# Kernel optimization log

Hardware: AMD Instinct MI355X
Metric: run time of the kernel (lower is better)

Reference implementation:

```python
import jax, jax.numpy as jnp
import numpy as np

EPS = 1e-20
TEMP = 0.07
HEAD_DIM = 128


def setup_inputs() -> dict:
    key = jax.random.key(0)
    k1, k2, k3 = jax.random.split(key, 3)
    B, C, T, H, W = 4, 512, 8, 32, 32
    x = jax.random.normal(k1, (B, C, T, H, W), dtype=jnp.float32)
    W_head = jax.random.normal(k2, (C, HEAD_DIM), dtype=jnp.float32) / np.sqrt(C).astype(np.float32)
    b_head = jax.random.normal(k3, (HEAD_DIM,), dtype=jnp.float32) * 0.01
    return {"x": x, "W_head": W_head, "b_head": b_head}


def _forward(x, W_head, b_head):
    B, C, T, H, W = x.shape
    N = H * W
    # linear head over channel dim (equivalent to permute->Linear->permute)
    feats = jnp.einsum('bcthw,cd->bdthw', x, W_head) + b_head[None, :, None, None, None]
    keys = feats.reshape(B, HEAD_DIM, T, N)
    # F.normalize(p=2, dim=1): x / max(||x||, 1e-12)
    norm = jnp.maximum(jnp.linalg.norm(keys, axis=1, keepdims=True), 1e-12)
    keys = keys / norm
    # affinity between consecutive frames: [B, T-1, N, N]
    A = jnp.einsum('bctn,bctm->btnm', keys[:, :, :-1], keys[:, :, 1:])
    A12 = jax.nn.softmax(A / TEMP, axis=-1)                         # forward stochastic mats
    A21 = jax.nn.softmax(jnp.swapaxes(A, -1, -2) / TEMP, axis=-1)   # backward stochastic mats
    A12s = jnp.swapaxes(A12, 0, 1)  # [T-1, B, N, N]
    A21s = jnp.swapaxes(A21, 0, 1)  # [T-1, B, N, N]

    # prefix products P[i] = A12[0] @ A12[1] @ ... @ A12[i]
    def step_p(carry, a):
        c = carry @ a
        return c, c
    _, Ptail = jax.lax.scan(step_p, A12s[0], A12s[1:])
    P = jnp.concatenate([A12s[:1], Ptail], axis=0)  # [T-1, B, N, N]

    # suffix products S[i] = A21[i] @ A21[i-1] @ ... @ A21[0]
    def step_s(carry, a):
        c = a @ carry
        return c, c
    _, Stail = jax.lax.scan(step_s, A21s[0], A21s[1:])
    S = jnp.concatenate([A21s[:1], Stail], axis=0)  # [T-1, B, N, N]

    # cycle walks for i = 1..T-2: aar_i = P[i] @ S[i]
    aars = jnp.matmul(P[1:], S[1:])  # [T-2, B, N, N]
    logits = jnp.log(aars + EPS)
    # cross-entropy with identity targets: loss = logsumexp - logit[n, n]
    lse = jax.nn.logsumexp(logits, axis=-1)                  # [T-2, B, N]
    diag = jnp.diagonal(logits, axis1=-2, axis2=-1)          # [T-2, B, N]
    losses = jnp.mean(lse - diag, axis=(1, 2))               # [T-2]
    preds = jnp.argmax(logits, axis=-1)                      # [T-2, B, N]
    tgt = jnp.arange(N)[None, None, :]
    accs = jnp.mean((preds == tgt).astype(jnp.float32), axis=(1, 2))
    # original returns (loss_of_last_walk, diags); diags exposed as stacked arrays
    return losses[-1], losses, accs


def reference(x, W_head, b_head):
    return _forward(x, W_head, b_head)
```

## Files before the change

kernel.cpp:

```cpp
#include <hip/hip_runtime.h>
#include <cstdint>
#include <cstddef>

typedef unsigned short u16;
typedef unsigned long long u64;
using short8 = __attribute__((ext_vector_type(8))) short;
using f32x4  = __attribute__((ext_vector_type(4))) float;

#define KEXP 20.609929155556620f

__device__ __forceinline__ u16 f2bf(float f) {
  unsigned u = __float_as_uint(f);
  u += 0x7fffu + ((u >> 16) & 1u);
  return (u16)(u >> 16);
}
__device__ __forceinline__ float bf2f(u16 h) { return __uint_as_float(((unsigned)h) << 16); }

typedef const unsigned int GASu32 __attribute__((address_space(1)));
typedef unsigned int LASu32 __attribute__((address_space(3)));

__device__ __forceinline__ void gload16(const u16* src, u16* dstLds) {
  __builtin_amdgcn_global_load_lds((GASu32*)src, (LASu32*)dstLds, 16, 0, 0);
}

__global__ __launch_bounds__(256) void transpose_x(const float* __restrict__ x, u16* __restrict__ xT) {
  __shared__ float t[32][33];
  int b = blockIdx.z, c0 = blockIdx.y * 32, s0 = blockIdx.x * 32;
  int tid = threadIdx.x;
  int ci = tid >> 3, s4 = (tid & 7) * 4;
  float4 v = *(const float4*)(x + ((size_t)b * 512 + c0 + ci) * 8192 + s0 + s4);
  t[ci][s4 + 0] = v.x; t[ci][s4 + 1] = v.y; t[ci][s4 + 2] = v.z; t[ci][s4 + 3] = v.w;
  __syncthreads();
  int si = tid >> 3, c4 = (tid & 7) * 4;
  ushort4 o;
  o.x = f2bf(t[c4 + 0][si]); o.y = f2bf(t[c4 + 1][si]);
  o.z = f2bf(t[c4 + 2][si]); o.w = f2bf(t[c4 + 3][si]);
  *(ushort4*)(xT + ((size_t)b * 8192 + s0 + si) * 512 + c0 + c4) = o;
}

__global__ __launch_bounds__(256) void transpose_w(const float* __restrict__ W, u16* __restrict__ Wt) {
  int idx = blockIdx.x * 256 + threadIdx.x;
  int d = idx >> 9, c = idx & 511;
  Wt[idx] = f2bf(W[c * 128 + d]);
}

__global__ __launch_bounds__(256) void normalize_keys(u16* __restrict__ keys) {
  int wv = threadIdx.x >> 6, lane = threadIdx.x & 63;
  int row = blockIdx.x * 4 + wv;
  unsigned* p = (unsigned*)(keys + (size_t)row * 128) + lane;
  unsigned v = *p;
  float a = bf2f((u16)(v & 0xffffu)), b = bf2f((u16)(v >> 16));
  float s = a * a + b * b;
  #pragma unroll
  for (int m = 1; m < 64; m <<= 1) s += __shfl_xor(s, m, 64);
  float sc = 1.f / fmaxf(sqrtf(s), 1e-12f);
  *p = (unsigned)f2bf(a * sc) | ((unsigned)f2bf(b * sc) << 16);
}

__global__ __launch_bounds__(256) void reduce_sums(const float* __restrict__ rsEP, const float* __restrict__ csEP,
                                                   float* __restrict__ rsumE, float* __restrict__ csumE) {
  int idx = blockIdx.x * 256 + threadIdx.x;
  int which = idx >= 28672;
  int base = which ? idx - 28672 : idx;
  int z = base >> 10, r = base & 1023;
  const float* src = which ? csEP : rsEP;
  float s = 0.f;
  #pragma unroll
  for (int k = 0; k < 16; ++k) s += src[(size_t)z * 16384 + k * 1024 + r];
  (which ? csumE : rsumE)[z * 1024 + r] = s;
}

__global__ __launch_bounds__(256) void k3_t0(const u16* __restrict__ E, const float* __restrict__ rsum,
                                             const float* __restrict__ csum,
                                             u16* __restrict__ P0, u16* __restrict__ S0) {
  int b = blockIdx.z, r = blockIdx.x;
  int zE = b * 7;
  const u16* e = E + ((size_t)zE << 20) + (size_t)r * 1024;
  float rr = 1.f / rsum[zE * 1024 + r];
  int c = threadIdx.x * 4;
  ushort4 v = *(const ushort4*)(e + c);
  float4 cv = *(const float4*)(csum + zE * 1024 + c);
  ushort4 o1, o2;
  float v0 = bf2f(v.x), v1 = bf2f(v.y), v2 = bf2f(v.z), v3 = bf2f(v.w);
  o1.x = f2bf(v0 * rr); o1.y = f2bf(v1 * rr); o1.z = f2bf(v2 * rr); o1.w = f2bf(v3 * rr);
  o2.x = f2bf(v0 / cv.x); o2.y = f2bf(v1 / cv.y); o2.z = f2bf(v2 / cv.z); o2.w = f2bf(v3 / cv.w);
  size_t base = ((size_t)b << 20) + (size_t)r * 1024 + c;
  *(ushort4*)(P0 + base) = o1;
  *(ushort4*)(S0 + base) = o2;
}

__global__ __launch_bounds__(256) void k3_tr(const u16* __restrict__ E, const float* __restrict__ rsum,
                                             const float* __restrict__ csum,
                                             u16* __restrict__ Bp, u16* __restrict__ Bs) {
  __shared__ u16 t[64][66];
  int z = blockIdx.z; int b = z / 6, tt = z % 6 + 1;
  int zE = b * 7 + tt;
  int er0 = blockIdx.x * 64, ec0 = blockIdx.y * 64;
  const u16* e = E + ((size_t)zE << 20);
  int tid = threadIdx.x;
  int ri = tid >> 4, c4 = (tid & 15) * 4;
  #pragma unroll
  for (int p = 0; p < 4; ++p) {
    ushort4 v = *(const ushort4*)(e + (size_t)(er0 + ri + p * 16) * 1024 + ec0 + c4);
    t[ri + p * 16][c4 + 0] = v.x; t[ri + p * 16][c4 + 1] = v.y;
    t[ri + p * 16][c4 + 2] = v.z; t[ri + p * 16][c4 + 3] = v.w;
  }
  __syncthreads();
  size_t outBase = (size_t)(b * 6 + tt - 1) << 20;
  float ir0 = 1.f / rsum[zE * 1024 + er0 + c4 + 0];
  float ir1 = 1.f / rsum[zE * 1024 + er0 + c4 + 1];
  float ir2 = 1.f / rsum[zE * 1024 + er0 + c4 + 2];
  float ir3 = 1.f / rsum[zE * 1024 + er0 + c4 + 3];
  #pragma unroll
  for (int p = 0; p < 4; ++p) {
    int roL = ri + p * 16;
    int ro = ec0 + roL;
    float ic = 1.f / csum[zE * 1024 + ro];
    float v0 = bf2f(t[c4 + 0][roL]), v1 = bf2f(t[c4 + 1][roL]);
    float v2 = bf2f(t[c4 + 2][roL]), v3 = bf2f(t[c4 + 3][roL]);
    ushort4 op, os;
    op.x = f2bf(v0 * ir0); op.y = f2bf(v1 * ir1); op.z = f2bf(v2 * ir2); op.w = f2bf(v3 * ir3);
    os.x = f2bf(v0 * ic);  os.y = f2bf(v1 * ic);  os.z = f2bf(v2 * ic);  os.w = f2bf(v3 * ic);
    size_t off = outBase + (size_t)ro * 1024 + er0 + c4;
    *(ushort4*)(Bp + off) = op;
    *(ushort4*)(Bs + off) = os;
  }
}

struct GemmBatch { const u16* A[24]; const u16* B[24]; u16* C[8]; };
enum { M_HEAD = 0, M_EXP = 1, M_PLAIN = 2, M_AAR = 3 };

__device__ __forceinline__ int lds_off32(int r, int kbyte) {
  int rp = r >> 1;
  int sl = (((r & 1) << 2) | (kbyte >> 4)) ^ (rp & 7);
  return rp * 128 + sl * 16;
}

#define GEMM_BODY(T, FA, FB, NA, NB)                                                    \
  {                                                                                     \
    int t_ = (T);                                                                       \
    if (t_ + 1 < nt) {                                                                  \
      if (t_ + 2 < nt) asm volatile("s_waitcnt vmcnt(4)" ::: "memory");                 \
      else             asm volatile("s_waitcnt vmcnt(0)" ::: "memory");                 \
      __builtin_amdgcn_s_barrier();                                                     \
      __builtin_amdgcn_sched_barrier(0);                                                \
      _Pragma("unroll")                                                                 \
      for (int f = 0; f < 4; ++f) {                                                     \
        NA[f] = *(const short8*)((const char*)An + offA[f]);                            \
        NB[f] = *(const short8*)((const char*)Bn + offB[f]);                            \
      }                                                                                 \
      if (t_ + 3 < nt) {                                                                \
        int k0_ = (t_ + 3) << 5;                                                        \
        gload16(srcA0 + k0_, A3 + ldso0);                                               \
        gload16(srcA1 + k0_, A3 + ldso1);                                               \
        gload16(srcB0 + k0_, B3 + ldso0);                                               \
        gload16(srcB1 + k0_, B3 + ldso1);                                               \
      }                                                                                 \
      asm volatile("s_waitcnt lgkmcnt(8)" ::: "memory");                                \
    } else {                                                                            \
      asm volatile("s_waitcnt lgkmcnt(0)" ::: "memory");                                \
    }                                                                                   \
    __builtin_amdgcn_sched_barrier(0);                                                  \
    __builtin_amdgcn_s_setprio(1);                                                      \
    _Pragma("unroll")                                                                   \
    for (int fr = 0; fr < 4; ++fr)                                                      \
      _Pragma("unroll")                                                                 \
      for (int fc2 = 0; fc2 < 4; ++fc2)                                                 \
        acc[fr][fc2] = __builtin_amdgcn_mfma_f32_16x16x32_bf16(FA[fr], FB[fc2],         \
                                                               acc[fr][fc2], 0, 0, 0); \
    __builtin_amdgcn_s_setprio(0);                                                      \
    { u16* tA = Ac; Ac = An; An = A2; A2 = A3; A3 = tA;                                 \
      u16* tB = Bc; Bc = Bn; Bn = B2; B2 = B3; B3 = tB; }                               \
  }

template <int MODE>
__global__ __launch_bounds__(256) void gemm_nt(const u16* __restrict__ gA, const u16* __restrict__ gB,
                                               u16* __restrict__ gC, GemmBatch batch,
                                               const float* __restrict__ bias,
                                               float* __restrict__ rsP, u64* __restrict__ amP,
                                               float* __restrict__ diagv,
                                               float* __restrict__ rsEP, float* __restrict__ csEP) {
  __shared__ u16 AsL[4][4096];
  __shared__ u16 BsL[4][4096];
  int tid = threadIdx.x, lane = tid & 63, wv = tid >> 6;
  int wr = wv >> 1, wc = wv & 1;
  int l15 = lane & 15, kb = (lane >> 4) << 4;

  int swz;
  { int per = (int)gridDim.x >> 3; int id0 = blockIdx.x; swz = (id0 & 7) * per + (id0 >> 3); }
  int z, m0, n0;
  if constexpr (MODE == M_HEAD) { z = 0; m0 = swz << 7; n0 = 0; }
  else { z = swz >> 6; int r6 = swz & 63; m0 = (r6 & 7) << 7; n0 = (r6 >> 3) << 7; }

  const u16 *A, *B; u16* C;
  int K, lda, ldb, ldc;
  if constexpr (MODE == M_HEAD) {
    A = gA; B = gB; C = gC; K = 512; lda = 512; ldb = 512; ldc = 128;
  } else if constexpr (MODE == M_EXP) {
    int b = z / 7, t = z % 7;
    size_t offA0 = (size_t)(b * 8 + t) * 131072;
    A = gA + offA0; B = gA + offA0 + 131072; C = gC + ((size_t)z << 20);
    K = 128; lda = 128; ldb = 128; ldc = 1024;
  } else if constexpr (MODE == M_PLAIN) {
    A = batch.A[z]; B = batch.B[z]; C = batch.C[z];
    K = 1024; lda = 1024; ldb = 1024; ldc = 1024;
  } else {
    A = batch.A[z]; B = batch.B[z]; C = nullptr;
    K = 1024; lda = 1024; ldb = 1024; ldc = 1024;
  }

  const u16 *srcA0, *srcA1, *srcB0, *srcB1;
  int ldso0, ldso1;
  {
    int g0 = tid, g1 = 256 + tid;
    int rp0 = g0 >> 3, sp0 = (g0 & 7) ^ (rp0 & 7);
    int r0_ = (rp0 << 1) | (sp0 >> 2), kb0 = (sp0 & 3) * 8;
    int rp1 = g1 >> 3, sp1 = (g1 & 7) ^ (rp1 & 7);
    int r1_ = (rp1 << 1) | (sp1 >> 2), kb1 = (sp1 & 3) * 8;
    srcA0 = A + (size_t)(m0 + r0_) * lda + kb0;
    srcA1 = A + (size_t)(m0 + r1_) * lda + kb1;
    srcB0 = B + (size_t)(n0 + r0_) * ldb + kb0;
    srcB1 = B + (size_t)(n0 + r1_) * ldb + kb1;
    ldso0 = g0 * 8; ldso1 = g1 * 8;
  }
  int offA[4], offB[4];
  #pragma unroll
  for (int f = 0; f < 4; ++f) {
    offA[f] = lds_off32((wr << 6) + (f << 4) + l15, kb);
    offB[f] = lds_off32((wc << 6) + (f << 4) + l15, kb);
  }

  f32x4 acc[4][4] = {};
  int nt = K >> 5;

  u16 *Ac = AsL[0], *An = AsL[1], *A2 = AsL[2], *A3 = AsL[3];
  u16 *Bc = BsL[0], *Bn = BsL[1], *B2 = BsL[2], *B3 = BsL[3];

  gload16(srcA0 +  0, Ac + ldso0); gload16(srcA1 +  0, Ac + ldso1);
  gload16(srcB0 +  0, Bc + ldso0); gload16(srcB1 +  0, Bc + ldso1);
  gload16(srcA0 + 32, An + ldso0); gload16(srcA1 + 32, An + ldso1);
  gload16(srcB0 + 32, Bn + ldso0); gload16(srcB1 + 32, Bn + ldso1);
  gload16(srcA0 + 64, A2 + ldso0); gload16(srcA1 + 64, A2 + ldso1);
  gload16(srcB0 + 64, B2 + ldso0); gload16(srcB1 + 64, B2 + ldso1);
  asm volatile("s_waitcnt vmcnt(8)" ::: "memory");
  __builtin_amdgcn_s_barrier();
  __builtin_amdgcn_sched_barrier(0);
  short8 fa0[4], fb0[4], fa1[4], fb1[4];
  #pragma unroll
  for (int f = 0; f < 4; ++f) {
    fa0[f] = *(const short8*)((const char*)Ac + offA[f]);
    fb0[f] = *(const short8*)((const char*)Bc + offB[f]);
  }

  for (int t = 0; t < nt; t += 2) {
    GEMM_BODY(t,     fa0, fb0, fa1, fb1);
    GEMM_BODY(t + 1, fa1, fb1, fa0, fb0);
  }

  if constexpr (MODE == M_AAR) {
    int nb = n0 >> 7;
    size_t pbase = (size_t)z * 16384 + (size_t)((nb << 1) | wc) * 1024;
    #pragma unroll
    for (int fr = 0; fr < 4; ++fr) {
      #pragma unroll
      for (int j = 0; j < 4; ++j) {
        float rs = 0.f, mv = -1.f; int mc = 0;
        #pragma unroll
        for (int fc = 0; fc < 4; ++fc) {
          float v = acc[fr][fc][j];
          rs += v;
          int c = n0 + (wc << 6) + (fc << 4) + l15;
          if (v > mv) { mv = v; mc = c; }
        }
        u64 pk = ((u64)__float_as_uint(mv) << 32) | (u64)(unsigned)(1023 - mc);
        #pragma unroll
        for (int m = 1; m < 16; m <<= 1) {
          rs += __shfl_xor(rs, m, 64);
          u64 o = __shfl_xor(pk, m, 64);
          pk = (o > pk) ? o : pk;
        }
        if (l15 == 0) {
          int row = m0 + (wr << 6) + (fr << 4) + ((lane >> 4) << 2) + j;
          rsP[pbase + row] = rs;
          amP[pbase + row] = pk;
        }
      }
      if (m0 == n0 && wr == wc) {
        int jj = l15 - ((lane >> 4) << 2);
        if (jj >= 0 && jj < 4) {
          int row = m0 + (wr << 6) + (fr << 4) + l15;
          float dv = (jj == 0) ? acc[fr][fr][0] : (jj == 1) ? acc[fr][fr][1]
                    : (jj == 2) ? acc[fr][fr][2] : acc[fr][fr][3];
          diagv[(z << 10) + row] = dv;
        }
      }
    }
  } else if constexpr (MODE == M_EXP) {
    float rp[4][4] = {};
    float cp[4] = {};
    #pragma unroll
    for (int fr = 0; fr < 4; ++fr)
      #pragma unroll
      for (int fc = 0; fc < 4; ++fc)
        #pragma unroll
        for (int j = 0; j < 4; ++j) {
          int row = m0 + (wr << 6) + (fr << 4) + ((lane >> 4) << 2) + j;
          int col = n0 + (wc << 6) + (fc << 4) + l15;
          float v = exp2f(acc[fr][fc][j] * KEXP);
          C[(size_t)row * ldc + col] = f2bf(v);
          rp[fr][j] += v;
          cp[fc] += v;
        }
    int nb = n0 >> 7, mb = m0 >> 7;
    size_t rbase = (size_t)z * 16384 + (size_t)((nb << 1) | wc) * 1024;
    size_t cbase = (size_t)z * 16384 + (size_t)((mb << 1) | wr) * 1024;
    #pragma unroll
    for (int fr = 0; fr < 4; ++fr)
      #pragma unroll
      for (int j = 0; j < 4; ++j) {
        float r = rp[fr][j];
        r += __shfl_xor(r, 1, 64); r += __shfl_xor(r, 2, 64);
        r += __shfl_xor(r, 4, 64); r += __shfl_xor(r, 8, 64);
        if (l15 == 0) {
          int row = m0 + (wr << 6) + (fr << 4) + ((lane >> 4) << 2) + j;
          rsEP[rbase + row] = r;
        }
      }
    #pragma unroll
    for (int fc = 0; fc < 4; ++fc) {
      float c = cp[fc];
      c += __shfl_xor(c, 16, 64); c += __shfl_xor(c, 32, 64);
      if ((lane >> 4) == 0) {
        int col = n0 + (wc << 6) + (fc << 4) + l15;
        csEP[cbase + col] = c;
      }
    }
  } else {
    #pragma unroll
    for (int fr = 0; fr < 4; ++fr)
      #pragma unroll
      for (int fc = 0; fc < 4; ++fc)
        #pragma unroll
        for (int j = 0; j < 4; ++j) {
          int row = m0 + (wr << 6) + (fr << 4) + ((lane >> 4) << 2) + j;
          int col = n0 + (wc << 6) + (fc << 4) + l15;
          float v = acc[fr][fc][j];
          if constexpr (MODE == M_HEAD) v += bias[col];
          C[(size_t)row * ldc + col] = f2bf(v);
        }
  }
}

__global__ __launch_bounds__(256) void finalize_k(const float* __restrict__ rsP, const u64* __restrict__ amP,
                                                  const float* __restrict__ diagv, float* __restrict__ out) {
  __shared__ float sl[256], sa[256];
  int w = blockIdx.x;
  int tid = threadIdx.x;
  float ls = 0.f, ac = 0.f;
  for (int idx = tid; idx < 4096; idx += 256) {
    int b = idx >> 10, n = idx & 1023;
    int z = (w << 2) + b;
    size_t base = (size_t)z * 16384 + n;
    float rs = 0.f; u64 pk = 0;
    #pragma unroll
    for (int k = 0; k < 16; ++k) {
      rs += rsP[base + k * 1024];
      u64 o = amP[base + k * 1024];
      pk = (o > pk) ? o : pk;
    }
    float dv = diagv[(z << 10) + n];
    ls += logf(rs + 1024.f * 1e-20f) - logf(dv + 1e-20f);
    unsigned pred = 1023u - (unsigned)(pk & 0xffffffffULL);
    ac += (pred == (unsigned)n) ? 1.f : 0.f;
  }
  sl[tid] = ls; sa[tid] = ac;
  __syncthreads();
  for (int s2 = 128; s2 > 0; s2 >>= 1) {
    if (tid < s2) { sl[tid] += sl[tid + s2]; sa[tid] += sa[tid + s2]; }
    __syncthreads();
  }
  if (tid == 0) {
    float loss = sl[0] / 4096.f, acv = sa[0] / 4096.f;
    out[1 + w] = loss;
    out[7 + w] = acv;
    if (w == 5) out[0] = loss;
  }
}

extern "C" void kernel_launch(void* const* d_in, const int* in_sizes, int n_in,
                              void* d_out, int out_size, void* d_ws, size_t ws_size,
                              hipStream_t stream) {
  (void)in_sizes; (void)n_in; (void)out_size; (void)ws_size;
  const float* x  = (const float*)d_in[0];
  const float* Wh = (const float*)d_in[1];
  const float* bh = (const float*)d_in[2];
  float* out = (float*)d_out;
  char* ws = (char*)d_ws;
  const size_t MB = 1ull << 20;

  u16* xT   = (u16*)(ws);
  u16* keys = (u16*)(ws + 32 * MB);
  float* rsP   = (float*)(ws + 32 * MB);
  u64*   amP   = (u64*)(ws + 34 * MB);
  float* diagv = (float*)(ws + 38 * MB);
  u16* Wt   = (u16*)(ws + 40 * MB);
  float* rsumE = (float*)(ws + 40 * MB + 128 * 1024);
  float* csumE = (float*)(ws + 40 * MB + 256 * 1024);
  u16* E    = (u16*)(ws + 41 * MB);
  float* rsEP  = (float*)(ws + 113 * MB);
  float* csEP  = (float*)(ws + 115 * MB);
  u16* Bp   = (u16*)(ws + 113 * MB);
  u16* Bs   = (u16*)(ws + 161 * MB);

  u16* Pb[7] = { (u16*)(ws + 97 * MB), (u16*)(ws + 0 * MB), (u16*)(ws + 8 * MB),
                 (u16*)(ws + 16 * MB), (u16*)(ws + 24 * MB), (u16*)(ws + 41 * MB),
                 (u16*)(ws + 49 * MB) };
  u16* Sb[7] = { (u16*)(ws + 105 * MB), (u16*)(ws + 57 * MB), (u16*)(ws + 65 * MB),
                 (u16*)(ws + 73 * MB), (u16*)(ws + 81 * MB), (u16*)(ws + 89 * MB),
                 (u16*)(ws + 97 * MB) };

  GemmBatch empty{};

  transpose_x<<<dim3(256, 16, 4), 256, 0, stream>>>(x, xT);
  transpose_w<<<dim3(256), 256, 0, stream>>>(Wh, Wt);
  gemm_nt<M_HEAD><<<dim3(256), 256, 0, stream>>>(xT, Wt, keys, empty, bh,
                                                 nullptr, nullptr, nullptr, nullptr, nullptr);
  normalize_keys<<<dim3(8192), 256, 0, stream>>>(keys);
  gemm_nt<M_EXP><<<dim3(1792), 256, 0, stream>>>(keys, nullptr, E, empty, nullptr,
                                                 nullptr, nullptr, nullptr, rsEP, csEP);
  reduce_sums<<<dim3(224), 256, 0, stream>>>(rsEP, csEP, rsumE, csumE);
  k3_t0<<<dim3(1024, 1, 4), 256, 0, stream>>>(E, rsumE, csumE, Pb[0], Sb[0]);
  k3_tr<<<dim3(16, 16, 24), 256, 0, stream>>>(E, rsumE, csumE, Bp, Bs);

  for (int i = 1; i <= 6; ++i) {
    GemmBatch gb{};
    for (int b = 0; b < 4; ++b) {
      gb.A[b]     = Pb[i - 1] + (size_t)b * 1048576;
      gb.B[b]     = Bp + (size_t)(b * 6 + i - 1) * 1048576;
      gb.C[b]     = Pb[i] + (size_t)b * 1048576;
      gb.A[4 + b] = Sb[i - 1] + (size_t)b * 1048576;
      gb.B[4 + b] = Bs + (size_t)(b * 6 + i - 1) * 1048576;
      gb.C[4 + b] = Sb[i] + (size_t)b * 1048576;
    }
    gemm_nt<M_PLAIN><<<dim3(512), 256, 0, stream>>>(nullptr, nullptr, nullptr, gb, nullptr,
                                                    nullptr, nullptr, nullptr, nullptr, nullptr);
  }

  GemmBatch ga{};
  for (int i = 1; i <= 6; ++i)
    for (int b = 0; b < 4; ++b) {
      ga.A[(i - 1) * 4 + b] = Pb[i] + (size_t)b * 1048576;
      ga.B[(i - 1) * 4 + b] = Sb[i] + (size_t)b * 1048576;
    }
  gemm_nt<M_AAR><<<dim3(1536), 256, 0, stream>>>(nullptr, nullptr, nullptr, ga, nullptr,
                                                 rsP, amP, diagv, nullptr, nullptr);
  finalize_k<<<dim3(6), 256, 0, stream>>>(rsP, amP, diagv, out);
}
```

Measured before the change: 320.6 us.

## Enlarge GEMM tiles to 256x256 with 512-thread blocks and triple buffering

The batched bf16 GEMM moves from 128x128 tiles on 4 waves to 256x256 tiles on 8 waves, with each wave computing 128x64 (8x4 MFMA fragments). The LDS pipeline drops from four stages to three so the larger tiles fit, and the epilogue indexing for the exp, row/col-sum, argmax and diagonal outputs is rewritten for the new layout. The column-sum partials and reduce_sums shrink to 8 partials, and the head GEMM pads W to 256 columns with zeros. The aim is more data reuse per loaded byte. The cost is fewer blocks (128 for the plain GEMMs on a 256-CU part), more registers per thread, and a shallower prefetch depth.

```diff
diff --git a/kernel.cpp b/kernel.cpp
--- a/kernel.cpp
+++ b/kernel.cpp
@@ -41,7 +41,7 @@
 __global__ __launch_bounds__(256) void transpose_w(const float* __restrict__ W, u16* __restrict__ Wt) {
   int idx = blockIdx.x * 256 + threadIdx.x;
   int d = idx >> 9, c = idx & 511;
-  Wt[idx] = f2bf(W[c * 128 + d]);
+  Wt[idx] = (d < 128) ? f2bf(W[c * 128 + d]) : (u16)0;
 }
 
 __global__ __launch_bounds__(256) void normalize_keys(u16* __restrict__ keys) {
@@ -60,14 +60,20 @@
 __global__ __launch_bounds__(256) void reduce_sums(const float* __restrict__ rsEP, const float* __restrict__ csEP,
                                                    float* __restrict__ rsumE, float* __restrict__ csumE) {
   int idx = blockIdx.x * 256 + threadIdx.x;
-  int which = idx >= 28672;
-  int base = which ? idx - 28672 : idx;
-  int z = base >> 10, r = base & 1023;
-  const float* src = which ? csEP : rsEP;
-  float s = 0.f;
-  #pragma unroll
-  for (int k = 0; k < 16; ++k) s += src[(size_t)z * 16384 + k * 1024 + r];
-  (which ? csumE : rsumE)[z * 1024 + r] = s;
+  if (idx < 28672) {
+    int z = idx >> 10, r = idx & 1023;
+    float s = 0.f;
+    #pragma unroll
+    for (int k = 0; k < 16; ++k) s += rsEP[(size_t)z * 16384 + k * 1024 + r];
+    rsumE[z * 1024 + r] = s;
+  } else {
+    int b2 = idx - 28672;
+    int z = b2 >> 10, c = b2 & 1023;
+    float s = 0.f;
+    #pragma unroll
+    for (int k = 0; k < 8; ++k) s += csEP[(size_t)z * 8192 + k * 1024 + c];
+    csumE[z * 1024 + c] = s;
+  }
 }
 
 __global__ __launch_bounds__(256) void k3_t0(const u16* __restrict__ E, const float* __restrict__ rsum,
@@ -145,52 +151,49 @@
       __builtin_amdgcn_s_barrier();                                                     \
       __builtin_amdgcn_sched_barrier(0);                                                \
       _Pragma("unroll")                                                                 \
-      for (int f = 0; f < 4; ++f) {                                                     \
-        NA[f] = *(const short8*)((const char*)An + offA[f]);                            \
-        NB[f] = *(const short8*)((const char*)Bn + offB[f]);                            \
-      }                                                                                 \
+      for (int f = 0; f < 8; ++f) NA[f] = *(const short8*)((const char*)An + offA[f]);  \
+      _Pragma("unroll")                                                                 \
+      for (int f = 0; f < 4; ++f) NB[f] = *(const short8*)((const char*)Bn + offB[f]);  \
       if (t_ + 3 < nt) {                                                                \
         int k0_ = (t_ + 3) << 5;                                                        \
-        gload16(srcA0 + k0_, A3 + ldso0);                                               \
-        gload16(srcA1 + k0_, A3 + ldso1);                                               \
-        gload16(srcB0 + k0_, B3 + ldso0);                                               \
-        gload16(srcB1 + k0_, B3 + ldso1);                                               \
+        gload16(sA0 + k0_, Ac + d0); gload16(sA1 + k0_, Ac + d1);                       \
+        gload16(sB0 + k0_, Bc + d0); gload16(sB1 + k0_, Bc + d1);                       \
       }                                                                                 \
-      asm volatile("s_waitcnt lgkmcnt(8)" ::: "memory");                                \
+      asm volatile("s_waitcnt lgkmcnt(12)" ::: "memory");                               \
     } else {                                                                            \
       asm volatile("s_waitcnt lgkmcnt(0)" ::: "memory");                                \
     }                                                                                   \
     __builtin_amdgcn_sched_barrier(0);                                                  \
     __builtin_amdgcn_s_setprio(1);                                                      \
     _Pragma("unroll")                                                                   \
-    for (int fr = 0; fr < 4; ++fr)                                                      \
+    for (int fa = 0; fa < 8; ++fa)                                                      \
       _Pragma("unroll")                                                                 \
-      for (int fc2 = 0; fc2 < 4; ++fc2)                                                 \
-        acc[fr][fc2] = __builtin_amdgcn_mfma_f32_16x16x32_bf16(FA[fr], FB[fc2],         \
-                                                               acc[fr][fc2], 0, 0, 0); \
+      for (int fb = 0; fb < 4; ++fb)                                                    \
+        acc[fa][fb] = __builtin_amdgcn_mfma_f32_16x16x32_bf16(FA[fa], FB[fb],           \
+                                                              acc[fa][fb], 0, 0, 0);   \
     __builtin_amdgcn_s_setprio(0);                                                      \
-    { u16* tA = Ac; Ac = An; An = A2; A2 = A3; A3 = tA;                                 \
-      u16* tB = Bc; Bc = Bn; Bn = B2; B2 = B3; B3 = tB; }                               \
+    { u16* tA = Ac; Ac = An; An = A2; A2 = tA;                                          \
+      u16* tB = Bc; Bc = Bn; Bn = B2; B2 = tB; }                                        \
   }
 
 template <int MODE>
-__global__ __launch_bounds__(256) void gemm_nt(const u16* __restrict__ gA, const u16* __restrict__ gB,
-                                               u16* __restrict__ gC, GemmBatch batch,
-                                               const float* __restrict__ bias,
-                                               float* __restrict__ rsP, u64* __restrict__ amP,
-                                               float* __restrict__ diagv,
-                                               float* __restrict__ rsEP, float* __restrict__ csEP) {
-  __shared__ u16 AsL[4][4096];
-  __shared__ u16 BsL[4][4096];
+__global__ __launch_bounds__(512, 2) void gemm_nt(const u16* __restrict__ gA, const u16* __restrict__ gB,
+                                                  u16* __restrict__ gC, GemmBatch batch,
+                                                  const float* __restrict__ bias,
+                                                  float* __restrict__ rsP, u64* __restrict__ amP,
+                                                  float* __restrict__ diagv,
+                                                  float* __restrict__ rsEP, float* __restrict__ csEP) {
+  __shared__ u16 AsL[3][8192];
+  __shared__ u16 BsL[3][8192];
   int tid = threadIdx.x, lane = tid & 63, wv = tid >> 6;
-  int wr = wv >> 1, wc = wv & 1;
+  int wrM = wv >> 2, wrN = wv & 3;
   int l15 = lane & 15, kb = (lane >> 4) << 4;
 
   int swz;
   { int per = (int)gridDim.x >> 3; int id0 = blockIdx.x; swz = (id0 & 7) * per + (id0 >> 3); }
   int z, m0, n0;
-  if constexpr (MODE == M_HEAD) { z = 0; m0 = swz << 7; n0 = 0; }
-  else { z = swz >> 6; int r6 = swz & 63; m0 = (r6 & 7) << 7; n0 = (r6 >> 3) << 7; }
+  if constexpr (MODE == M_HEAD) { z = 0; m0 = swz << 8; n0 = 0; }
+  else { z = swz >> 4; int r4 = swz & 15; m0 = (r4 & 3) << 8; n0 = (r4 >> 2) << 8; }
 
   const u16 *A, *B; u16* C;
   int K, lda, ldb, ldc;
@@ -209,48 +212,45 @@
     K = 1024; lda = 1024; ldb = 1024; ldc = 1024;
   }
 
-  const u16 *srcA0, *srcA1, *srcB0, *srcB1;
-  int ldso0, ldso1;
+  const u16 *sA0, *sA1, *sB0, *sB1;
+  int d0 = tid * 8, d1 = (512 + tid) * 8;
   {
-    int g0 = tid, g1 = 256 + tid;
+    int g0 = tid, g1 = 512 + tid;
     int rp0 = g0 >> 3, sp0 = (g0 & 7) ^ (rp0 & 7);
     int r0_ = (rp0 << 1) | (sp0 >> 2), kb0 = (sp0 & 3) * 8;
     int rp1 = g1 >> 3, sp1 = (g1 & 7) ^ (rp1 & 7);
     int r1_ = (rp1 << 1) | (sp1 >> 2), kb1 = (sp1 & 3) * 8;
-    srcA0 = A + (size_t)(m0 + r0_) * lda + kb0;
-    srcA1 = A + (size_t)(m0 + r1_) * lda + kb1;
-    srcB0 = B + (size_t)(n0 + r0_) * ldb + kb0;
-    srcB1 = B + (size_t)(n0 + r1_) * ldb + kb1;
-    ldso0 = g0 * 8; ldso1 = g1 * 8;
-  }
-  int offA[4], offB[4];
-  #pragma unroll
-  for (int f = 0; f < 4; ++f) {
-    offA[f] = lds_off32((wr << 6) + (f << 4) + l15, kb);
-    offB[f] = lds_off32((wc << 6) + (f << 4) + l15, kb);
-  }
-
-  f32x4 acc[4][4] = {};
+    sA0 = A + (size_t)(m0 + r0_) * lda + kb0;
+    sA1 = A + (size_t)(m0 + r1_) * lda + kb1;
+    sB0 = B + (size_t)(n0 + r0_) * ldb + kb0;
+    sB1 = B + (size_t)(n0 + r1_) * ldb + kb1;
+  }
+  int offA[8], offB[4];
+  #pragma unroll
+  for (int f = 0; f < 8; ++f) offA[f] = lds_off32(wrM * 128 + f * 16 + l15, kb);
+  #pragma unroll
+  for (int f = 0; f < 4; ++f) offB[f] = lds_off32(wrN * 64 + f * 16 + l15, kb);
+
+  f32x4 acc[8][4] = {};
   int nt = K >> 5;
 
-  u16 *Ac = AsL[0], *An = AsL[1], *A2 = AsL[2], *A3 = AsL[3];
-  u16 *Bc = BsL[0], *Bn = BsL[1], *B2 = BsL[2], *B3 = BsL[3];
-
-  gload16(srcA0 +  0, Ac + ldso0); gload16(srcA1 +  0, Ac + ldso1);
-  gload16(srcB0 +  0, Bc + ldso0); gload16(srcB1 +  0, Bc + ldso1);
-  gload16(srcA0 + 32, An + ldso0); gload16(srcA1 + 32, An + ldso1);
-  gload16(srcB0 + 32, Bn + ldso0); gload16(srcB1 + 32, Bn + ldso1);
-  gload16(srcA0 + 64, A2 + ldso0); gload16(srcA1 + 64, A2 + ldso1);
-  gload16(srcB0 + 64, B2 + ldso0); gload16(srcB1 + 64, B2 + ldso1);
+  u16 *Ac = AsL[0], *An = AsL[1], *A2 = AsL[2];
+  u16 *Bc = BsL[0], *Bn = BsL[1], *B2 = BsL[2];
+
+  gload16(sA0,      Ac + d0); gload16(sA1,      Ac + d1);
+  gload16(sB0,      Bc + d0); gload16(sB1,      Bc + d1);
+  gload16(sA0 + 32, An + d0); gload16(sA1 + 32, An + d1);
+  gload16(sB0 + 32, Bn + d0); gload16(sB1 + 32, Bn + d1);
+  gload16(sA0 + 64, A2 + d0); gload16(sA1 + 64, A2 + d1);
+  gload16(sB0 + 64, B2 + d0); gload16(sB1 + 64, B2 + d1);
   asm volatile("s_waitcnt vmcnt(8)" ::: "memory");
   __builtin_amdgcn_s_barrier();
   __builtin_amdgcn_sched_barrier(0);
-  short8 fa0[4], fb0[4], fa1[4], fb1[4];
-  #pragma unroll
-  for (int f = 0; f < 4; ++f) {
-    fa0[f] = *(const short8*)((const char*)Ac + offA[f]);
-    fb0[f] = *(const short8*)((const char*)Bc + offB[f]);
-  }
+  short8 fa0[8], fb0[4], fa1[8], fb1[4];
+  #pragma unroll
+  for (int f = 0; f < 8; ++f) fa0[f] = *(const short8*)((const char*)Ac + offA[f]);
+  #pragma unroll
+  for (int f = 0; f < 4; ++f) fb0[f] = *(const short8*)((const char*)Bc + offB[f]);
 
   for (int t = 0; t < nt; t += 2) {
     GEMM_BODY(t,     fa0, fb0, fa1, fb1);
@@ -258,18 +258,18 @@
   }
 
   if constexpr (MODE == M_AAR) {
-    int nb = n0 >> 7;
-    size_t pbase = (size_t)z * 16384 + (size_t)((nb << 1) | wc) * 1024;
-    #pragma unroll
-    for (int fr = 0; fr < 4; ++fr) {
+    int nb = n0 >> 8;
+    size_t pbase = (size_t)z * 16384 + (size_t)((nb << 2) | wrN) * 1024;
+    #pragma unroll
+    for (int fa = 0; fa < 8; ++fa) {
       #pragma unroll
       for (int j = 0; j < 4; ++j) {
         float rs = 0.f, mv = -1.f; int mc = 0;
         #pragma unroll
-        for (int fc = 0; fc < 4; ++fc) {
-          float v = acc[fr][fc][j];
+        for (int fb = 0; fb < 4; ++fb) {
+          float v = acc[fa][fb][j];
           rs += v;
-          int c = n0 + (wc << 6) + (fc << 4) + l15;
+          int c = n0 + (wrN << 6) + (fb << 4) + l15;
           if (v > mv) { mv = v; mc = c; }
         }
         u64 pk = ((u64)__float_as_uint(mv) << 32) | (u64)(unsigned)(1023 - mc);
@@ -280,73 +280,88 @@
           pk = (o > pk) ? o : pk;
         }
         if (l15 == 0) {
-          int row = m0 + (wr << 6) + (fr << 4) + ((lane >> 4) << 2) + j;
+          int row = m0 + (wrM << 7) + (fa << 4) + ((lane >> 4) << 2) + j;
           rsP[pbase + row] = rs;
           amP[pbase + row] = pk;
         }
       }
-      if (m0 == n0 && wr == wc) {
+      if (m0 == n0 && wrN == ((wrM << 1) | (fa >> 2))) {
+        int fb = fa & 3;
         int jj = l15 - ((lane >> 4) << 2);
         if (jj >= 0 && jj < 4) {
-          int row = m0 + (wr << 6) + (fr << 4) + l15;
-          float dv = (jj == 0) ? acc[fr][fr][0] : (jj == 1) ? acc[fr][fr][1]
-                    : (jj == 2) ? acc[fr][fr][2] : acc[fr][fr][3];
+          int row = m0 + (wrM << 7) + (fa << 4) + l15;
+          float dv = (jj == 0) ? acc[fa][fb][0] : (jj == 1) ? acc[fa][fb][1]
+                    : (jj == 2) ? acc[fa][fb][2] : acc[fa][fb][3];
           diagv[(z << 10) + row] = dv;
         }
       }
     }
   } else if constexpr (MODE == M_EXP) {
-    float rp[4][4] = {};
-    float cp[4] = {};
-    #pragma unroll
-    for (int fr = 0; fr < 4; ++fr)
-      #pragma unroll
-      for (int fc = 0; fc < 4; ++fc)
+    float rp_[8][4] = {};
+    float cp_[4] = {};
+    #pragma unroll
+    for (int fa = 0; fa < 8; ++fa)
+      #pragma unroll
+      for (int fb = 0; fb < 4; ++fb)
         #pragma unroll
         for (int j = 0; j < 4; ++j) {
-          int row = m0 + (wr << 6) + (fr << 4) + ((lane >> 4) << 2) + j;
-          int col = n0 + (wc << 6) + (fc << 4) + l15;
-          float v = exp2f(acc[fr][fc][j] * KEXP);
+          int row = m0 + (wrM << 7) + (fa << 4) + ((lane >> 4) << 2) + j;
+          int col = n0 + (wrN << 6) + (fb << 4) + l15;
+          float v = exp2f(acc[fa][fb][j] * KEXP);
           C[(size_t)row * ldc + col] = f2bf(v);
-          rp[fr][j] += v;
-          cp[fc] += v;
-        }
-    int nb = n0 >> 7, mb = m0 >> 7;
-    size_t rbase = (size_t)z * 16384 + (size_t)((nb << 1) | wc) * 1024;
-    size_t cbase = (size_t)z * 16384 + (size_t)((mb << 1) | wr) * 1024;
-    #pragma unroll
-    for (int fr = 0; fr < 4; ++fr)
+          rp_[fa][j] += v;
+          cp_[fb] += v;
+        }
+    int nb = n0 >> 8, mb = m0 >> 8;
+    size_t rbase = (size_t)z * 16384 + (size_t)((nb << 2) | wrN) * 1024;
+    size_t cbase = (size_t)z * 8192 + (size_t)((mb << 1) | wrM) * 1024;
+    #pragma unroll
+    for (int fa = 0; fa < 8; ++fa)
       #pragma unroll
       for (int j = 0; j < 4; ++j) {
-        float r = rp[fr][j];
+        float r = rp_[fa][j];
         r += __shfl_xor(r, 1, 64); r += __shfl_xor(r, 2, 64);
         r += __shfl_xor(r, 4, 64); r += __shfl_xor(r, 8, 64);
         if (l15 == 0) {
-          int row = m0 + (wr << 6) + (fr << 4) + ((lane >> 4) << 2) + j;
+          int row = m0 + (wrM << 7) + (fa << 4) + ((lane >> 4) << 2) + j;
           rsEP[rbase + row] = r;
         }
       }
     #pragma unroll
-    for (int fc = 0; fc < 4; ++fc) {
-      float c = cp[fc];
+    for (int fb = 0; fb < 4; ++fb) {
+      float c = cp_[fb];
       c += __shfl_xor(c, 16, 64); c += __shfl_xor(c, 32, 64);
       if ((lane >> 4) == 0) {
-        int col = n0 + (wc << 6) + (fc << 4) + l15;
+        int col = n0 + (wrN << 6) + (fb << 4) + l15;
         csEP[cbase + col] = c;
       }
     }
+  } else if constexpr (MODE == M_HEAD) {
+    if (wrN < 2) {
+      float bv[4][16 / 16];
+      #pragma unroll
+      for (int fb = 0; fb < 4; ++fb) bv[fb][0] = bias[(wrN << 6) + (fb << 4) + l15];
+      #pragma unroll
+      for (int fa = 0; fa < 8; ++fa)
+        #pragma unroll
+        for (int fb = 0; fb < 4; ++fb)
+          #pragma unroll
+          for (int j = 0; j < 4; ++j) {
+            int row = m0 + (wrM << 7) + (fa << 4) + ((lane >> 4) << 2) + j;
+            int col = (wrN << 6) + (fb << 4) + l15;
+            C[(size_t)row * 128 + col] = f2bf(acc[fa][fb][j] + bv[fb][0]);
+          }
+    }
   } else {
     #pragma unroll
-    for (int fr = 0; fr < 4; ++fr)
-      #pragma unroll
-      for (int fc = 0; fc < 4; ++fc)
+    for (int fa = 0; fa < 8; ++fa)
+      #pragma unroll
+      for (int fb = 0; fb < 4; ++fb)
         #pragma unroll
         for (int j = 0; j < 4; ++j) {
-          int row = m0 + (wr << 6) + (fr << 4) + ((lane >> 4) << 2) + j;
-          int col = n0 + (wc << 6) + (fc << 4) + l15;
-          float v = acc[fr][fc][j];
-          if constexpr (MODE == M_HEAD) v += bias[col];
-          C[(size_t)row * ldc + col] = f2bf(v);
+          int row = m0 + (wrM << 7) + (fa << 4) + ((lane >> 4) << 2) + j;
+          int col = n0 + (wrN << 6) + (fb << 4) + l15;
+          C[(size_t)row * 1024 + col] = f2bf(acc[fa][fb][j]);
         }
   }
 }
@@ -403,12 +418,12 @@
   float* rsP   = (float*)(ws + 32 * MB);
   u64*   amP   = (u64*)(ws + 34 * MB);
   float* diagv = (float*)(ws + 38 * MB);
-  u16* Wt   = (u16*)(ws + 40 * MB);
-  float* rsumE = (float*)(ws + 40 * MB + 128 * 1024);
-  float* csumE = (float*)(ws + 40 * MB + 256 * 1024);
+  u16* WtP  = (u16*)(ws + 40 * MB);
+  float* rsumE = (float*)(ws + 40 * MB + 288 * 1024);
+  float* csumE = (float*)(ws + 40 * MB + 416 * 1024);
   u16* E    = (u16*)(ws + 41 * MB);
   float* rsEP  = (float*)(ws + 113 * MB);
-  float* csEP  = (float*)(ws + 115 * MB);
+  float* csEP  = (float*)(ws + 116 * MB);
   u16* Bp   = (u16*)(ws + 113 * MB);
   u16* Bs   = (u16*)(ws + 161 * MB);
 
@@ -422,12 +437,12 @@
   GemmBatch empty{};
 
   transpose_x<<<dim3(256, 16, 4), 256, 0, stream>>>(x, xT);
-  transpose_w<<<dim3(256), 256, 0, stream>>>(Wh, Wt);
-  gemm_nt<M_HEAD><<<dim3(256), 256, 0, stream>>>(xT, Wt, keys, empty, bh,
+  transpose_w<<<dim3(512), 256, 0, stream>>>(Wh, WtP);
+  gemm_nt<M_HEAD><<<dim3(128), 512, 0, stream>>>(xT, WtP, keys, empty, bh,
                                                  nullptr, nullptr, nullptr, nullptr, nullptr);
   normalize_keys<<<dim3(8192), 256, 0, stream>>>(keys);
-  gemm_nt<M_EXP><<<dim3(1792), 256, 0, stream>>>(keys, nullptr, E, empty, nullptr,
-                                                 nullptr, nullptr, nullptr, rsEP, csEP);
+  gemm_nt<M_EXP><<<dim3(448), 512, 0, stream>>>(keys, nullptr, E, empty, nullptr,
+                                                nullptr, nullptr, nullptr, rsEP, csEP);
   reduce_sums<<<dim3(224), 256, 0, stream>>>(rsEP, csEP, rsumE, csumE);
   k3_t0<<<dim3(1024, 1, 4), 256, 0, stream>>>(E, rsumE, csumE, Pb[0], Sb[0]);
   k3_tr<<<dim3(16, 16, 24), 256, 0, stream>>>(E, rsumE, csumE, Bp, Bs);
@@ -442,7 +457,7 @@
       gb.B[4 + b] = Bs + (size_t)(b * 6 + i - 1) * 1048576;
       gb.C[4 + b] = Sb[i] + (size_t)b * 1048576;
     }
-    gemm_nt<M_PLAIN><<<dim3(512), 256, 0, stream>>>(nullptr, nullptr, nullptr, gb, nullptr,
+    gemm_nt<M_PLAIN><<<dim3(128), 512, 0, stream>>>(nullptr, nullptr, nullptr, gb, nullptr,
                                                     nullptr, nullptr, nullptr, nullptr, nullptr);
   }
 
@@ -452,7 +467,7 @@
       ga.A[(i - 1) * 4 + b] = Pb[i] + (size_t)b * 1048576;
       ga.B[(i - 1) * 4 + b] = Sb[i] + (size_t)b * 1048576;
     }
-  gemm_nt<M_AAR><<<dim3(1536), 256, 0, stream>>>(nullptr, nullptr, nullptr, ga, nullptr,
-                                                 rsP, amP, diagv, nullptr, nullptr);
+  gemm_nt<M_AAR><<<dim3(384), 512, 0, stream>>>(nullptr, nullptr, nullptr, ga, nullptr,
+                                                rsP, amP, diagv, nullptr, nullptr);
   finalize_k<<<dim3(6), 256, 0, stream>>>(rsP, amP, diagv, out);
 }
```

After: 387.2 us. +20.8%, slower.
